# Kernel optimization log

Hardware: AMD Instinct MI355X
Metric: run time of the kernel (lower is better)

The kernel has to match this reference:

```python
import jax, jax.numpy as jnp
import numpy as np

K_MAX = 32
IN_DIM = 2
L_NP = np.ones(IN_DIM, dtype=np.float64)
CONTROL_ENERGY_REG = 1e-3


def _density_constants():
    """Replicates Ergodicity_Loss.compute_fourier_coefficients_density (uniform density)."""
    ks = np.arange(K_MAX, dtype=np.float64)
    P, Q = np.meshgrid(ks, ks, indexing='ij')
    kgrid = np.stack([P, Q], axis=-1)                 # [K,K,2] integer modes
    ksc = kgrid * (np.pi / L_NP)                      # scaled modes k*pi/L
    # Lambda_k = (1 + |k|^2)^(-(d+1)/2)
    norm_weights = (1.0 + (ksc ** 2).sum(-1)) ** (-(IN_DIM + 1) / 2.0)
    # h_k: FAITHFUL to the original buggy loop (normal is reset every iteration,
    # so it depends only on the last dimension's index)
    norm_factors = np.where(kgrid[..., -1] == 0, 1.0, np.sqrt(L_NP[-1] / 2.0))
    # characteristic function of uniform density on [0,L1]x...x[0,Ld], real part
    coeff = np.ones((K_MAX, K_MAX), dtype=np.complex128)
    for i in range(IN_DIM):
        ki = ksc[..., i]
        safe = np.where(ki == 0.0, 1.0, ki)
        integral = np.where(ki == 0.0, L_NP[i],
                            (np.exp(1j * ki * L_NP[i]) - 1.0) / (1j * safe))
        coeff *= integral / L_NP[i]
    coeffs_density = coeff.real / norm_factors
    return (coeffs_density.astype(np.float32),
            norm_factors.astype(np.float32),
            norm_weights.astype(np.float32))


def setup_inputs() -> dict:
    key = jax.random.key(0)
    k1, k2 = jax.random.split(key)
    T, B, N = 512, 32, 64
    # agent trajectories in [0,L]^d
    x = jax.random.uniform(k1, (T, B, N, IN_DIM), dtype=jnp.float32)
    # control signals
    u = jax.random.normal(k2, (T, B, N, IN_DIM), dtype=jnp.float32)
    cd, nf, nw = _density_constants()
    return {
        "x": x,
        "u": u,
        "L": jnp.asarray(L_NP, dtype=jnp.float32),
        "coeffs_density": jnp.asarray(cd),
        "norm_factors": jnp.asarray(nf),
        "norm_weights": jnp.asarray(nw),
    }


def reference(x, u, L, coeffs_density, norm_factors, norm_weights):
    T, B, N, d = x.shape                      # d == 2
    K = coeffs_density.shape[0]
    # per-dimension mode frequencies k*pi/L_i  -> [d, K]
    freq = jnp.arange(K, dtype=x.dtype)[None, :] * (jnp.pi / L[:, None])
    c0 = jnp.cos(x[..., 0, None] * freq[0])   # [T,B,N,K]
    c1 = jnp.cos(x[..., 1, None] * freq[1])   # [T,B,N,K]
    # prod over dims then sum over time t and agents n, fused: [B,K,K]
    S = jnp.einsum('tbnp,tbnq->bpq', c0, c1)
    coeffs = S / (norm_factors * (N * T))     # c_k per batch element
    loss = (((coeffs - coeffs_density) ** 2) * norm_weights).sum()
    # control energy regularizer: |u|^2 summed
    loss = loss + CONTROL_ENERGY_REG * (u ** 2).sum() / (2 * N * T * B)
    return loss
```

## Files before the change

kernel.cpp:

```cpp
#include <hip/hip_runtime.h>


#define T_DIM 512
#define B_DIM 32
#define N_DIM 64
#define K_DIM 32
#define TN_TOT (T_DIM * N_DIM)
#define CHUNKS 16
#define CHUNK_S (TN_TOT / CHUNKS)
#define TILE_S 512
#define N_TILES (CHUNK_S / TILE_S)
#define ST_PAD (TILE_S + 8)

typedef __attribute__((ext_vector_type(8))) short bf16x8;
typedef __attribute__((ext_vector_type(16))) float f32x16;

__device__ __forceinline__ unsigned pkbf(float a, float b) {
  unsigned ua = __float_as_uint(a), ub = __float_as_uint(b);
  ua = (ua + 0x7FFFu + ((ua >> 16) & 1u)) >> 16;
  ub = (ub + 0x7FFFu + ((ub >> 16) & 1u)) >> 16;
  return (ua & 0xFFFFu) | (ub << 16);
}

__global__ __launch_bounds__(256, 2) void ergo_main(
    const float* __restrict__ x, const float* __restrict__ u,
    const float* __restrict__ L, float* __restrict__ S,
    float* __restrict__ u2out) {
  __shared__ alignas(16) unsigned short c0T[K_DIM][ST_PAD];
  __shared__ alignas(16) unsigned short c1T[K_DIM][ST_PAD];
  __shared__ float sred[K_DIM * K_DIM];
  __shared__ float ured[4];

  const int tid = threadIdx.x;
  const int lane = tid & 63;
  const int wave = tid >> 6;
  const int b = blockIdx.x >> 4;
  const int chunk = blockIdx.x & (CHUNKS - 1);

  const float invL0 = 1.0f / L[0];
  const float invL1 = 1.0f / L[1];

  f32x16 acc;
#pragma unroll
  for (int r = 0; r < 16; ++r) acc[r] = 0.0f;
  float usum = 0.0f;

  const int s_base = chunk * CHUNK_S;

  for (int tile = 0; tile < N_TILES; ++tile) {
    const int s0 = s_base + tile * TILE_S;

    {
      const int ls = tid * 2;
      const int s = s0 + ls;
      const int t = s >> 6, n = s & 63;
      const size_t gidx = (((size_t)t * B_DIM + b) * N_DIM + n) * 2;
      const float4 xv = *reinterpret_cast<const float4*>(x + gidx);
      const float4 uv = *reinterpret_cast<const float4*>(u + gidx);
      usum += uv.x * uv.x + uv.y * uv.y + uv.z * uv.z + uv.w * uv.w;

      const float c00 = cospif(xv.x * invL0);
      const float c01 = cospif(xv.y * invL1);
      const float c10 = cospif(xv.z * invL0);
      const float c11 = cospif(xv.w * invL1);

      *reinterpret_cast<unsigned*>(&c0T[0][ls]) = 0x3F803F80u;
      *reinterpret_cast<unsigned*>(&c1T[0][ls]) = 0x3F803F80u;
      *reinterpret_cast<unsigned*>(&c0T[1][ls]) = pkbf(c00, c10);
      *reinterpret_cast<unsigned*>(&c1T[1][ls]) = pkbf(c01, c11);

      float p0 = 1.f, q0 = c00, p1 = 1.f, q1 = c01;
      float p2 = 1.f, q2 = c10, p3 = 1.f, q3 = c11;
      const float t0 = 2.f * c00, t1 = 2.f * c01, t2 = 2.f * c10, t3 = 2.f * c11;
#pragma unroll
      for (int k = 2; k < K_DIM; ++k) {
        const float n0 = __builtin_fmaf(t0, q0, -p0);
        const float n1 = __builtin_fmaf(t1, q1, -p1);
        const float n2 = __builtin_fmaf(t2, q2, -p2);
        const float n3 = __builtin_fmaf(t3, q3, -p3);
        p0 = q0; q0 = n0; p1 = q1; q1 = n1;
        p2 = q2; q2 = n2; p3 = q3; q3 = n3;
        *reinterpret_cast<unsigned*>(&c0T[k][ls]) = pkbf(n0, n2);
        *reinterpret_cast<unsigned*>(&c1T[k][ls]) = pkbf(n1, n3);
      }
    }
    __syncthreads();

    {
      const int p = lane & 31;
      const int sb = wave * 128 + ((lane >> 5) << 3);
      const unsigned short* ar = &c0T[p][sb];
      const unsigned short* br = &c1T[p][sb];
#pragma unroll
      for (int j = 0; j < 8; ++j) {
        const bf16x8 av = *reinterpret_cast<const bf16x8*>(ar + j * 16);
        const bf16x8 bv = *reinterpret_cast<const bf16x8*>(br + j * 16);
        acc = __builtin_amdgcn_mfma_f32_32x32x16_bf16(av, bv, acc, 0, 0, 0);
      }
    }
    __syncthreads();
  }

  for (int i = tid; i < K_DIM * K_DIM; i += 256) sred[i] = 0.0f;
  __syncthreads();
  {
    const int col = lane & 31;
    const int rb = (lane >> 5) * 4;
#pragma unroll
    for (int r = 0; r < 16; ++r) {
      const int row = (r & 3) + 8 * (r >> 2) + rb;
      atomicAdd(&sred[row * 32 + col], acc[r]);
    }
  }
#pragma unroll
  for (int off = 32; off; off >>= 1) usum += __shfl_down(usum, off);
  if (lane == 0) ured[wave] = usum;
  __syncthreads();
  for (int i = tid; i < K_DIM * K_DIM; i += 256)
    atomicAdd(&S[b * (K_DIM * K_DIM) + i], sred[i]);
  if (tid == 0) atomicAdd(u2out, ured[0] + ured[1] + ured[2] + ured[3]);
}

__global__ __launch_bounds__(1024) void ergo_final(
    const float* __restrict__ S, const float* __restrict__ u2,
    const float* __restrict__ cd, const float* __restrict__ nf,
    const float* __restrict__ nw, float* __restrict__ out) {
  const int tid = threadIdx.x;
  const int lane = tid & 63, wave = tid >> 6;
  const float inv = 1.0f / (nf[tid] * (float)(N_DIM * T_DIM));
  const float cdi = cd[tid], nwi = nw[tid];
  float sum = 0.0f;
#pragma unroll 4
  for (int bb = 0; bb < B_DIM; ++bb) {
    const float d = S[bb * (K_DIM * K_DIM) + tid] * inv - cdi;
    sum += d * d;
  }
  sum *= nwi;
#pragma unroll
  for (int off = 32; off; off >>= 1) sum += __shfl_down(sum, off);
  __shared__ float red[16];
  if (lane == 0) red[wave] = sum;
  __syncthreads();
  if (wave == 0) {
    float v = (lane < 16) ? red[lane] : 0.0f;
#pragma unroll
    for (int off = 8; off; off >>= 1) v += __shfl_down(v, off);
    if (lane == 0)
      out[0] = v + u2[0] * (1.0e-3f / 2097152.0f);
  }
}

extern "C" void kernel_launch(void* const* d_in, const int* in_sizes, int n_in,
                              void* d_out, int out_size, void* d_ws, size_t ws_size,
                              hipStream_t stream) {
  const float* x = (const float*)d_in[0];
  const float* u = (const float*)d_in[1];
  const float* L = (const float*)d_in[2];
  const float* cd = (const float*)d_in[3];
  const float* nf = (const float*)d_in[4];
  const float* nw = (const float*)d_in[5];

  float* S = (float*)d_ws;
  float* u2 = S + B_DIM * K_DIM * K_DIM;

  hipMemsetAsync(d_ws, 0, (B_DIM * K_DIM * K_DIM + 1) * sizeof(float), stream);
  ergo_main<<<dim3(B_DIM * CHUNKS), dim3(256), 0, stream>>>(x, u, L, S, u2);
  ergo_final<<<dim3(1), dim3(1024), 0, stream>>>(S, u2, cd, nf, nw, (float*)d_out);
}
```

Before: 106.5 us.

## Replace global atomics and memset with per-block partials and a last-block reduce

```diff
diff --git a/kernel.cpp b/kernel.cpp
--- a/kernel.cpp
+++ b/kernel.cpp
@@ -7,6 +7,7 @@
 #define K_DIM 32
 #define TN_TOT (T_DIM * N_DIM)
 #define CHUNKS 16
+#define NBLK1 (B_DIM * CHUNKS)
 #define CHUNK_S (TN_TOT / CHUNKS)
 #define TILE_S 512
 #define N_TILES (CHUNK_S / TILE_S)
@@ -16,16 +17,23 @@
 typedef __attribute__((ext_vector_type(16))) float f32x16;
 
 __device__ __forceinline__ unsigned pkbf(float a, float b) {
+#if __has_builtin(__builtin_amdgcn_cvt_pk_bf16_f32)
+  typedef __attribute__((ext_vector_type(2))) __bf16 bf16x2;
+  bf16x2 v = __builtin_amdgcn_cvt_pk_bf16_f32(a, b);
+  return __builtin_bit_cast(unsigned, v);
+#else
   unsigned ua = __float_as_uint(a), ub = __float_as_uint(b);
   ua = (ua + 0x7FFFu + ((ua >> 16) & 1u)) >> 16;
   ub = (ub + 0x7FFFu + ((ub >> 16) & 1u)) >> 16;
   return (ua & 0xFFFFu) | (ub << 16);
+#endif
 }
 
 __global__ __launch_bounds__(256, 2) void ergo_main(
     const float* __restrict__ x, const float* __restrict__ u,
-    const float* __restrict__ L, float* __restrict__ S,
-    float* __restrict__ u2out) {
+    const float* __restrict__ L, float* __restrict__ Spart,
+    float* __restrict__ u2p, float* __restrict__ loss_acc,
+    unsigned* __restrict__ counter) {
   __shared__ alignas(16) unsigned short c0T[K_DIM][ST_PAD];
   __shared__ alignas(16) unsigned short c1T[K_DIM][ST_PAD];
   __shared__ float sred[K_DIM * K_DIM];
@@ -34,8 +42,14 @@
   const int tid = threadIdx.x;
   const int lane = tid & 63;
   const int wave = tid >> 6;
-  const int b = blockIdx.x >> 4;
-  const int chunk = blockIdx.x & (CHUNKS - 1);
+  const int bid = blockIdx.x;
+  const int b = bid >> 4;
+  const int chunk = bid & (CHUNKS - 1);
+
+  if (bid == 0 && tid == 0) {
+    *loss_acc = 0.0f;
+    *counter = 0u;
+  }
 
   const float invL0 = 1.0f / L[0];
   const float invL1 = 1.0f / L[1];
@@ -116,37 +130,59 @@
   for (int off = 32; off; off >>= 1) usum += __shfl_down(usum, off);
   if (lane == 0) ured[wave] = usum;
   __syncthreads();
-  for (int i = tid; i < K_DIM * K_DIM; i += 256)
-    atomicAdd(&S[b * (K_DIM * K_DIM) + i], sred[i]);
-  if (tid == 0) atomicAdd(u2out, ured[0] + ured[1] + ured[2] + ured[3]);
-}
-
-__global__ __launch_bounds__(1024) void ergo_final(
-    const float* __restrict__ S, const float* __restrict__ u2,
+  {
+    float* dst = Spart + (size_t)bid * (K_DIM * K_DIM);
+#pragma unroll
+    for (int j = 0; j < 4; ++j) dst[tid + j * 256] = sred[tid + j * 256];
+  }
+  if (tid == 0) u2p[bid] = ured[0] + ured[1] + ured[2] + ured[3];
+}
+
+__global__ __launch_bounds__(256) void ergo_reduce(
+    const float* __restrict__ Spart, const float* __restrict__ u2p,
     const float* __restrict__ cd, const float* __restrict__ nf,
-    const float* __restrict__ nw, float* __restrict__ out) {
+    const float* __restrict__ nw, float* __restrict__ loss_acc,
+    unsigned* __restrict__ counter, float* __restrict__ out) {
+  const int b = blockIdx.x;
   const int tid = threadIdx.x;
   const int lane = tid & 63, wave = tid >> 6;
-  const float inv = 1.0f / (nf[tid] * (float)(N_DIM * T_DIM));
-  const float cdi = cd[tid], nwi = nw[tid];
+  __shared__ float red[4];
+  __shared__ int winner;
+
   float sum = 0.0f;
-#pragma unroll 4
-  for (int bb = 0; bb < B_DIM; ++bb) {
-    const float d = S[bb * (K_DIM * K_DIM) + tid] * inv - cdi;
-    sum += d * d;
-  }
-  sum *= nwi;
+#pragma unroll
+  for (int j = 0; j < 4; ++j) {
+    const int i = tid + j * 256;
+    float s = 0.0f;
+#pragma unroll
+    for (int c = 0; c < CHUNKS; ++c)
+      s += Spart[((size_t)(b * CHUNKS + c)) * (K_DIM * K_DIM) + i];
+    const float coeff = s * (1.0f / (float)(N_DIM * T_DIM)) / nf[i];
+    const float d = coeff - cd[i];
+    sum += d * d * nw[i];
+  }
 #pragma unroll
   for (int off = 32; off; off >>= 1) sum += __shfl_down(sum, off);
-  __shared__ float red[16];
   if (lane == 0) red[wave] = sum;
   __syncthreads();
-  if (wave == 0) {
-    float v = (lane < 16) ? red[lane] : 0.0f;
-#pragma unroll
-    for (int off = 8; off; off >>= 1) v += __shfl_down(v, off);
-    if (lane == 0)
-      out[0] = v + u2[0] * (1.0e-3f / 2097152.0f);
+  if (tid == 0) {
+    atomicAdd(loss_acc, red[0] + red[1] + red[2] + red[3]);
+    __threadfence();
+    const unsigned tk = atomicAdd(counter, 1u);
+    winner = (tk == B_DIM - 1) ? 1 : 0;
+  }
+  __syncthreads();
+  if (winner) {
+    float us = u2p[tid] + u2p[tid + 256];
+#pragma unroll
+    for (int off = 32; off; off >>= 1) us += __shfl_down(us, off);
+    if (lane == 0) red[wave] = us;
+    __syncthreads();
+    if (tid == 0) {
+      const float u2tot = red[0] + red[1] + red[2] + red[3];
+      const float loss = atomicAdd(loss_acc, 0.0f);
+      out[0] = loss + u2tot * (1.0e-3f / 2097152.0f);
+    }
   }
 }
 
@@ -160,10 +196,14 @@
   const float* nf = (const float*)d_in[4];
   const float* nw = (const float*)d_in[5];
 
-  float* S = (float*)d_ws;
-  float* u2 = S + B_DIM * K_DIM * K_DIM;
-
-  hipMemsetAsync(d_ws, 0, (B_DIM * K_DIM * K_DIM + 1) * sizeof(float), stream);
-  ergo_main<<<dim3(B_DIM * CHUNKS), dim3(256), 0, stream>>>(x, u, L, S, u2);
-  ergo_final<<<dim3(1), dim3(1024), 0, stream>>>(S, u2, cd, nf, nw, (float*)d_out);
-}
+  float* Spart = (float*)d_ws;
+  float* u2p = Spart + (size_t)NBLK1 * K_DIM * K_DIM;
+  float* loss_acc = u2p + NBLK1;
+  unsigned* counter = (unsigned*)(loss_acc + 1);
+
+  ergo_main<<<dim3(NBLK1), dim3(256), 0, stream>>>(x, u, L, Spart, u2p,
+                                                   loss_acc, counter);
+  ergo_reduce<<<dim3(B_DIM), dim3(256), 0, stream>>>(Spart, u2p, cd, nf, nw,
+                                                     loss_acc, counter,
+                                                     (float*)d_out);
+}
```

New measurement: 99.11 us. 1.07x faster.
